# Optimization experiments

Hardware: AMD Instinct MI355X
Metric: run time of the kernel (lower is better)

The kernel has to match this reference:

```python
import jax, jax.numpy as jnp
import numpy as np

B, L = 8, 2048          # images, lines per image
C_IN, HW = 256, 128     # backbone feature channels, spatial size
DIM_LOI = 128
N_PTS0, N_PTS1 = 32, 8  # sampled points per line, after maxpool
SCALE = N_PTS0 // N_PTS1
EPS = 1e-5


def setup_inputs() -> dict:
    key = jax.random.key(0)
    ks = jax.random.split(key, 24)
    d = {}
    d['feature'] = jax.random.normal(ks[0], (B, C_IN, HW, HW), jnp.float32)
    # line endpoints in pixel coords [0, 128)
    d['lines'] = jax.random.uniform(ks[1], (B, L, 2, 2), jnp.float32) * HW
    # fc1: 1x1 conv 256 -> 128
    d['fc1_w'] = jax.random.normal(ks[2], (DIM_LOI, C_IN), jnp.float32) * 0.05
    d['fc1_b'] = jnp.zeros((DIM_LOI,), jnp.float32)
    planes = DIM_LOI // 2
    def bn(k, c):
        k1, k2, k3 = jax.random.split(k, 3)
        return (jax.random.normal(k1, (c,), jnp.float32) * 0.1 + 1.0,
                jax.random.normal(k2, (c,), jnp.float32) * 0.1,
                jax.random.normal(k3, (c,), jnp.float32) * 0.05,
                jax.random.uniform(jax.random.fold_in(k, 7), (c,), jnp.float32, 0.5, 1.5))
    d['bn1_g'], d['bn1_b'], d['bn1_m'], d['bn1_v'] = bn(ks[3], DIM_LOI)
    d['conv1_w'] = jax.random.normal(ks[4], (planes, DIM_LOI), jnp.float32) * 0.05
    d['conv1_b'] = jnp.zeros((planes,), jnp.float32)
    d['bn2_g'], d['bn2_b'], d['bn2_m'], d['bn2_v'] = bn(ks[5], planes)
    d['conv2_w'] = jax.random.normal(ks[6], (planes, planes, 3), jnp.float32) * 0.05
    d['conv2_b'] = jnp.zeros((planes,), jnp.float32)
    d['bn3_g'], d['bn3_b'], d['bn3_m'], d['bn3_v'] = bn(ks[7], planes)
    d['conv3_w'] = jax.random.normal(ks[8], (DIM_LOI, planes), jnp.float32) * 0.05
    d['conv3_b'] = jnp.zeros((DIM_LOI,), jnp.float32)
    d['fc2_w'] = jax.random.normal(ks[9], (1, DIM_LOI * N_PTS1), jnp.float32) * 0.02
    d['fc2_b'] = jnp.zeros((1,), jnp.float32)
    return d


def _bn(x, g, b, m, v):
    # x: [N, C, T], eval-mode batchnorm
    s = g * jax.lax.rsqrt(v + EPS)
    return x * s[None, :, None] + (b - m * s)[None, :, None]


def _loi_forward(feature, lines, fc1_w, fc1_b,
                 bn1_g, bn1_b, bn1_m, bn1_v, conv1_w, conv1_b,
                 bn2_g, bn2_b, bn2_m, bn2_v, conv2_w, conv2_b,
                 bn3_g, bn3_b, bn3_m, bn3_v, conv3_w, conv3_b,
                 fc2_w, fc2_b):
    # fc1: 1x1 conv -> [B, DIM_LOI, H, W]
    x = jnp.einsum('oc,bchw->bohw', fc1_w, feature) + fc1_b[None, :, None, None]

    # sample N_PTS0 points per line: p = p0*lam + p1*(1-lam) - 0.5
    lam = jnp.linspace(0.0, 1.0, N_PTS0, dtype=lines.dtype)  # [P]
    pts = (lines[:, :, 0, None, :] * lam[None, None, :, None]
           + lines[:, :, 1, None, :] * (1.0 - lam[None, None, :, None]) - 0.5)  # [B,L,P,2]
    px, py = pts[..., 0], pts[..., 1]
    px0 = jnp.clip(jnp.floor(px), 0.0, HW - 1.0)
    py0 = jnp.clip(jnp.floor(py), 0.0, HW - 1.0)
    px1 = jnp.clip(px0 + 1.0, 0.0, HW - 1.0)
    py1 = jnp.clip(py0 + 1.0, 0.0, HW - 1.0)
    px0l, py0l = px0.astype(jnp.int32), py0.astype(jnp.int32)
    px1l, py1l = px1.astype(jnp.int32), py1.astype(jnp.int32)

    def gather(f, ix, iy):  # f: [C,H,W], ix/iy: [L,P] -> [C,L,P]
        return f[:, ix, iy]

    gat = jax.vmap(gather)  # over batch
    xp = (gat(x, px0l, py0l) * ((px1 - px) * (py1 - py))[:, None]
          + gat(x, px1l, py0l) * ((px - px0) * (py1 - py))[:, None]
          + gat(x, px0l, py1l) * ((px1 - px) * (py - py0))[:, None]
          + gat(x, px1l, py1l) * ((px - px0) * (py - py0))[:, None])  # [B,C,L,P]

    xp = xp.transpose(0, 2, 1, 3).reshape(B * L, DIM_LOI, N_PTS0)  # [N,C,P]
    # MaxPool1d(kernel=stride=SCALE)
    xp = xp.reshape(B * L, DIM_LOI, N_PTS1, SCALE).max(axis=-1)  # [N,C,T=8]

    # Bottleneck1D residual: x + op(x)
    h = jax.nn.relu(_bn(xp, bn1_g, bn1_b, bn1_m, bn1_v))
    h = jnp.einsum('oc,nct->not', conv1_w, h) + conv1_b[None, :, None]
    h = jax.nn.relu(_bn(h, bn2_g, bn2_b, bn2_m, bn2_v))
    h = jax.lax.conv_general_dilated(h, conv2_w, (1,), [(1, 1)],
                                     dimension_numbers=('NCH', 'OIH', 'NCH'))
    h = h + conv2_b[None, :, None]
    h = jax.nn.relu(_bn(h, bn3_g, bn3_b, bn3_m, bn3_v))
    h = jnp.einsum('oc,nct->not', conv3_w, h) + conv3_b[None, :, None]
    xp = xp + h

    # fc2: ReLU -> Linear(dim_loi*n_pts1, 1)
    flat = jax.nn.relu(xp).reshape(B * L, DIM_LOI * N_PTS1)
    logits = (flat @ fc2_w.T + fc2_b).reshape(-1)  # [B*L]
    return logits


def reference(feature, lines, fc1_w, fc1_b,
              bn1_g, bn1_b, bn1_m, bn1_v, conv1_w, conv1_b,
              bn2_g, bn2_b, bn2_m, bn2_v, conv2_w, conv2_b,
              bn3_g, bn3_b, bn3_m, bn3_v, conv3_w, conv3_b,
              fc2_w, fc2_b):
    return _loi_forward(feature, lines, fc1_w, fc1_b,
                        bn1_g, bn1_b, bn1_m, bn1_v, conv1_w, conv1_b,
                        bn2_g, bn2_b, bn2_m, bn2_v, conv2_w, conv2_b,
                        bn3_g, bn3_b, bn3_m, bn3_v, conv3_w, conv3_b,
                        fc2_w, fc2_b)
```

## Files before the change

### kernel.cpp

```cpp
#include <hip/hip_runtime.h>

#define EPSBN 1e-5f

typedef _Float16 f16;
typedef _Float16 f16x8 __attribute__((ext_vector_type(8)));
typedef _Float16 f16x4 __attribute__((ext_vector_type(4)));
typedef _Float16 f16x2 __attribute__((ext_vector_type(2)));
typedef float    f32x4 __attribute__((ext_vector_type(4)));

#define AS1 __attribute__((address_space(1)))
#define AS3 __attribute__((address_space(3)))

__device__ inline f16x8 hmax8(f16x8 a, f16x8 b) {
    f16x8 r;
    #pragma unroll
    for (int i = 0; i < 8; ++i) r[i] = a[i] > b[i] ? a[i] : b[i];
    return r;
}
__device__ inline f16x8 relu8(f16x8 v) {
    f16x8 r;
    #pragma unroll
    for (int i = 0; i < 8; ++i) r[i] = v[i] > (f16)0.f ? v[i] : (f16)0.f;
    return r;
}

__global__ void wprep_kernel(const float* __restrict__ fc1w,
                             const float* __restrict__ w1,
                             const float* __restrict__ w2,
                             const float* __restrict__ w3,
                             f16* __restrict__ dst) {
    const int i = blockIdx.x * 256 + threadIdx.x;
    float v;
    if (i < 32768) {
        const int k8 = i & 7, otg = (i >> 3) & 7, l = (i >> 6) & 63, s = i >> 12;
        const int n16l = l & 15, quadl = l >> 4;
        v = fc1w[(otg * 16 + n16l) * 256 + s * 32 + quadl * 8 + k8];
    }
    else if (i < 40960) v = w1[i - 32768];
    else if (i < 53248) {
        const int j = i - 40960, tau = j >> 12, rest = j & 4095;
        v = w2[rest * 3 + tau];
    } else              v = w3[i - 53248];
    dst[i] = (f16)v;
}

__global__ __launch_bounds__(1024, 4)
void fc1_mfma(const float* __restrict__ feat,
              const f16*   __restrict__ wfrag,
              const float* __restrict__ bias,
              f16*         __restrict__ xmap) {
    __shared__ f16 wlds[32768];
    __shared__ union {
        f16 xb[2][32][264];
        f16 epi[128][132];
    } u;

    const int tid  = threadIdx.x;
    const int wv   = tid >> 6;
    const int lane = tid & 63;
    const int n16  = lane & 15, quad = lane >> 4;
    const int pw   = wv >> 1;
    const int ow   = wv & 1;
    const int img  = blockIdx.x & 7;
    const int p0   = (blockIdx.x >> 3) << 8;

    const float* fimg = feat + (((size_t)img) << 22);

    const int sch = tid >> 5, sg = tid & 31;
    const float* sbase = fimg + (((size_t)sch) << 14) + p0 + sg * 8;

    f32x4 acc[2][4];
    #pragma unroll
    for (int ptg = 0; ptg < 2; ++ptg)
        #pragma unroll
        for (int t = 0; t < 4; ++t) acc[ptg][t] = (f32x4){0.f, 0.f, 0.f, 0.f};

    #pragma unroll
    for (int c4 = 0; c4 < 4; ++c4) {
        const int c = wv + 16 * c4;
        __builtin_amdgcn_global_load_lds((const AS1 void*)(wfrag + c * 512 + lane * 8),
                                         (AS3 void*)(wlds + c * 512), 16, 0, 0);
    }
    float4 st[2][2];
    st[0][0] = *(const float4*)(sbase);
    st[0][1] = *(const float4*)(sbase + 4);
    st[1][0] = *(const float4*)(sbase + 524288);
    st[1][1] = *(const float4*)(sbase + 524292);
    {
        f16x8 h;
        #pragma unroll
        for (int i = 0; i < 4; ++i) { h[i] = (f16)st[0][0][i]; h[i + 4] = (f16)st[0][1][i]; }
        *(f16x8*)&u.xb[0][sch][sg * 8] = h;
    }
    asm volatile("s_waitcnt vmcnt(0)" ::: "memory");
    __syncthreads();

    #pragma unroll
    for (int s = 0; s < 8; ++s) {
        if (s < 6) {
            st[s & 1][0] = *(const float4*)(sbase + (size_t)(s + 2) * 524288);
            st[s & 1][1] = *(const float4*)(sbase + (size_t)(s + 2) * 524288 + 4);
        }

        f16x8 wf[4];
        #pragma unroll
        for (int t = 0; t < 4; ++t)
            wf[t] = *(const f16x8*)&wlds[((s * 64 + lane) * 8 + ow * 4 + t) * 8];

        f16x8 xf[2];
        #pragma unroll
        for (int ptg = 0; ptg < 2; ++ptg) {
            const int pt = pw * 32 + ptg * 16 + n16;
            f16x8 xv;
            #pragma unroll
            for (int j = 0; j < 8; ++j) xv[j] = u.xb[s & 1][quad * 8 + j][pt];
            xf[ptg] = xv;
        }

        #pragma unroll
        for (int ptg = 0; ptg < 2; ++ptg)
            #pragma unroll
            for (int t = 0; t < 4; ++t)
                acc[ptg][t] = __builtin_amdgcn_mfma_f32_16x16x32_f16(wf[t], xf[ptg],
                                                                     acc[ptg][t], 0, 0, 0);

        if (s < 7) {
            f16x8 h;
            #pragma unroll
            for (int i = 0; i < 4; ++i) {
                h[i]     = (f16)st[(s + 1) & 1][0][i];
                h[i + 4] = (f16)st[(s + 1) & 1][1][i];
            }
            *(f16x8*)&u.xb[(s + 1) & 1][sch][sg * 8] = h;

            __builtin_amdgcn_sched_barrier(0);
            asm volatile("s_waitcnt lgkmcnt(0)" ::: "memory");
            __builtin_amdgcn_sched_barrier(0);
            __builtin_amdgcn_s_barrier();
            __builtin_amdgcn_sched_barrier(0);
        }
    }

    #pragma unroll
    for (int P = 0; P < 2; ++P) {
        __syncthreads();
        if ((pw >> 2) == P) {
            #pragma unroll
            for (int ptg = 0; ptg < 2; ++ptg) {
                const int rowl = (pw & 3) * 32 + ptg * 16 + n16;
                #pragma unroll
                for (int t = 0; t < 4; ++t) {
                    const int o = ow * 64 + t * 16 + quad * 4;
                    const float4 bq = *(const float4*)&bias[o];
                    f16x4 hv;
                    hv[0] = (f16)(acc[ptg][t][0] + bq.x);
                    hv[1] = (f16)(acc[ptg][t][1] + bq.y);
                    hv[2] = (f16)(acc[ptg][t][2] + bq.z);
                    hv[3] = (f16)(acc[ptg][t][3] + bq.w);
                    *(f16x4*)&u.epi[rowl][o] = hv;
                }
            }
        }
        __syncthreads();
        #pragma unroll
        for (int it = 0; it < 2; ++it) {
            const int idx = it * 1024 + tid;
            const int rowl = idx >> 4, seg = idx & 15;
            const float4 v = *(const float4*)&u.epi[rowl][seg * 8];
            *(float4*)&xmap[(((size_t)(img * 16384 + p0 + P * 128 + rowl)) << 7) + seg * 8] = v;
        }
    }
}

__global__ __launch_bounds__(256)
void loi_kernel(const f16*   __restrict__ x,
                const float* __restrict__ lines,
                const f16*   __restrict__ wsp,
                const float* __restrict__ bn1g, const float* __restrict__ bn1b,
                const float* __restrict__ bn1m, const float* __restrict__ bn1v,
                const float* __restrict__ b1,
                const float* __restrict__ bn2g, const float* __restrict__ bn2b,
                const float* __restrict__ bn2m, const float* __restrict__ bn2v,
                const float* __restrict__ b2,
                const float* __restrict__ bn3g, const float* __restrict__ bn3b,
                const float* __restrict__ bn3m, const float* __restrict__ bn3v,
                const float* __restrict__ b3,
                const float* __restrict__ fc2w, const float* __restrict__ fc2b,
                float* __restrict__ out) {
    __shared__ f16 xp[64][136];
    __shared__ alignas(16) union {
        struct { int toff[256][4]; f16 twgt[256][4]; } tp;
        struct { f16 h1[80][72]; f16 h2[64][72]; } cv;
    } u;
    __shared__ f16 s1h[128], t1h[128];
    __shared__ float s2f[64], t2f[64], s3f[64], t3f[64], b1f[64], b2f[64];
    __shared__ float b3f[128];
    __shared__ float wsum[4][8];

    const f16* w1f16 = wsp + 32768;
    const f16* w2f16 = wsp + 40960;
    const f16* w3f16 = wsp + 53248;

    const int tid  = threadIdx.x;
    const int wv   = tid >> 6, lane = tid & 63;
    const int n16  = lane & 15, quad = lane >> 4;
    const int img  = blockIdx.x & 7;
    const int mblk = blockIdx.x >> 3;

    if (tid < 128) {
        const float s = bn1g[tid] * rsqrtf(bn1v[tid] + EPSBN);
        s1h[tid] = (f16)s; t1h[tid] = (f16)(bn1b[tid] - bn1m[tid] * s);
    }
    if (tid < 64) {
        const float s = bn2g[tid] * rsqrtf(bn2v[tid] + EPSBN);
        s2f[tid] = s; t2f[tid] = bn2b[tid] - bn2m[tid] * s;
        b1f[tid] = b1[tid];
    } else if (tid < 128) {
        const int c = tid - 64;
        const float s = bn3g[c] * rsqrtf(bn3v[c] + EPSBN);
        s3f[c] = s; t3f[c] = bn3b[c] - bn3m[c] * s;
        b2f[c] = b2[c];
    } else {
        b3f[tid - 128] = b3[tid - 128];
    }

    {
        const int li = tid >> 5, pt = tid & 31;
        const int gl = img * 2048 + mblk * 8 + li;
        const float4 ln = *(const float4*)&lines[gl * 4];
        const float lam = (float)pt * (1.0f / 31.0f);
        const float px = ln.x * lam + ln.z * (1.f - lam) - 0.5f;
        const float py = ln.y * lam + ln.w * (1.f - lam) - 0.5f;
        const float px0 = fminf(fmaxf(floorf(px), 0.f), 127.f);
        const float py0 = fminf(fmaxf(floorf(py), 0.f), 127.f);
        const float px1 = fminf(px0 + 1.f, 127.f);
        const float py1 = fminf(py0 + 1.f, 127.f);
        const int ix0 = (int)px0, iy0 = (int)py0;
        const int ix1 = (int)px1, iy1 = (int)py1;
        u.tp.toff[tid][0] = (((ix0 << 7) + iy0) << 7);
        u.tp.toff[tid][1] = (((ix1 << 7) + iy0) << 7);
        u.tp.toff[tid][2] = (((ix0 << 7) + iy1) << 7);
        u.tp.toff[tid][3] = (((ix1 << 7) + iy1) << 7);
        const float wx1 = px1 - px, wx0 = px - px0;
        const float wy1 = py1 - py, wy0 = py - py0;
        u.tp.twgt[tid][0] = (f16)(wx1 * wy1); u.tp.twgt[tid][1] = (f16)(wx0 * wy1);
        u.tp.twgt[tid][2] = (f16)(wx1 * wy0); u.tp.twgt[tid][3] = (f16)(wx0 * wy0);
    }
    __syncthreads();

    {
        const int h  = lane >> 5;
        const int sh = (lane >> 4) & 1;
        const int j  = lane & 15;
        const int li = wv * 2 + h;
        const f16* xbh = x + (((size_t)img) << 21) + 8 * j;
        #pragma unroll
        for (int t = 0; t < 8; ++t) {
            f16x8 m;
            #pragma unroll
            for (int q = 0; q < 8; ++q) m[q] = (f16)(-60000.f);
            #pragma unroll
            for (int ss = 0; ss < 2; ++ss) {
                const int combo = li * 32 + t * 4 + sh * 2 + ss;
                const int4  off = *(const int4*)&u.tp.toff[combo][0];
                const f16x4 tw  = *(const f16x4*)&u.tp.twgt[combo][0];
                const f16x8 g00 = *(const f16x8*)(xbh + off.x);
                const f16x8 g10 = *(const f16x8*)(xbh + off.y);
                const f16x8 g01 = *(const f16x8*)(xbh + off.z);
                const f16x8 g11 = *(const f16x8*)(xbh + off.w);
                f16x8 w0, w1v, w2v, w3v;
                #pragma unroll
                for (int q = 0; q < 8; ++q) {
                    w0[q] = tw[0]; w1v[q] = tw[1]; w2v[q] = tw[2]; w3v[q] = tw[3];
                }
                const f16x8 v = g00 * w0 + g10 * w1v + g01 * w2v + g11 * w3v;
                m = hmax8(m, v);
            }
            union { f16x8 v8; int i4[4]; } cv;
            cv.v8 = m;
            #pragma unroll
            for (int q = 0; q < 4; ++q) cv.i4[q] = __shfl_xor(cv.i4[q], 16, 64);
            m = hmax8(m, cv.v8);
            if (sh == 0) *(f16x8*)&xp[li * 8 + t][8 * j] = m;
        }
    }
    __syncthreads();

    {
        const int r = tid >> 4, seg = tid & 15;
        const int row = (r >> 1) * 10 + (r & 1) * 9;
        *(unsigned long long*)&u.cv.h1[row][seg * 4] = 0ull;
    }

    {
        const int o_lane = wv * 16 + n16;
        f32x4 acc1[4];
        #pragma unroll
        for (int nt = 0; nt < 4; ++nt) acc1[nt] = (f32x4){0.f, 0.f, 0.f, 0.f};
        #pragma unroll
        for (int ks = 0; ks < 4; ++ks) {
            const int k = ks * 32 + quad * 8;
            const f16x8 a  = *(const f16x8*)&w1f16[o_lane * 128 + k];
            const f16x8 s8 = *(const f16x8*)&s1h[k];
            const f16x8 t8 = *(const f16x8*)&t1h[k];
            #pragma unroll
            for (int nt = 0; nt < 4; ++nt) {
                const f16x8 raw = *(const f16x8*)&xp[nt * 16 + n16][k];
                const f16x8 bf = relu8(raw * s8 + t8);
                acc1[nt] = __builtin_amdgcn_mfma_f32_16x16x32_f16(a, bf, acc1[nt], 0, 0, 0);
            }
        }
        #pragma unroll
        for (int nt = 0; nt < 4; ++nt) {
            const int n = nt * 16 + n16;
            const int nprow = (n >> 3) * 10 + (n & 7) + 1;
            #pragma unroll
            for (int r = 0; r < 4; ++r) {
                const int o = wv * 16 + quad * 4 + r;
                const float v = fmaxf((acc1[nt][r] + b1f[o]) * s2f[o] + t2f[o], 0.f);
                u.cv.h1[nprow][o] = (f16)v;
            }
        }
    }
    __syncthreads();

    {
        const int o_lane = wv * 16 + n16;
        f32x4 acc2[4];
        #pragma unroll
        for (int nt = 0; nt < 4; ++nt) acc2[nt] = (f32x4){0.f, 0.f, 0.f, 0.f};
        #pragma unroll
        for (int d = 0; d < 3; ++d) {
            const f16* A2 = w2f16 + d * 4096;
            #pragma unroll
            for (int ks = 0; ks < 2; ++ks) {
                const int k = ks * 32 + quad * 8;
                const f16x8 a = *(const f16x8*)&A2[o_lane * 64 + k];
                #pragma unroll
                for (int nt = 0; nt < 4; ++nt) {
                    const int n = nt * 16 + n16;
                    const int row = (n >> 3) * 10 + (n & 7) + d;
                    const f16x8 bf = *(const f16x8*)&u.cv.h1[row][k];
                    acc2[nt] = __builtin_amdgcn_mfma_f32_16x16x32_f16(a, bf, acc2[nt], 0, 0, 0);
                }
            }
        }
        #pragma unroll
        for (int nt = 0; nt < 4; ++nt) {
            const int n = nt * 16 + n16;
            #pragma unroll
            for (int r = 0; r < 4; ++r) {
                const int o = wv * 16 + quad * 4 + r;
                const float v = fmaxf((acc2[nt][r] + b2f[o]) * s3f[o] + t3f[o], 0.f);
                u.cv.h2[n][o] = (f16)v;
            }
        }
    }
    __syncthreads();

    {
        const int col = n16 & 7, obase = wv * 16 + quad * 4;
        float fcv[2][4];
        #pragma unroll
        for (int h = 0; h < 2; ++h)
            #pragma unroll
            for (int r = 0; r < 4; ++r)
                fcv[h][r] = fc2w[(h * 64 + obase + r) * 8 + col];

        f32x4 acc3[2][4];
        #pragma unroll
        for (int h = 0; h < 2; ++h)
            #pragma unroll
            for (int nt = 0; nt < 4; ++nt) acc3[h][nt] = (f32x4){0.f, 0.f, 0.f, 0.f};
        #pragma unroll
        for (int ks = 0; ks < 2; ++ks) {
            const int k = ks * 32 + quad * 8;
            const f16x8 a0 = *(const f16x8*)&w3f16[(wv * 16 + n16) * 64 + k];
            const f16x8 a1 = *(const f16x8*)&w3f16[(64 + wv * 16 + n16) * 64 + k];
            #pragma unroll
            for (int nt = 0; nt < 4; ++nt) {
                const f16x8 bf = *(const f16x8*)&u.cv.h2[nt * 16 + n16][k];
                acc3[0][nt] = __builtin_amdgcn_mfma_f32_16x16x32_f16(a0, bf, acc3[0][nt], 0, 0, 0);
                acc3[1][nt] = __builtin_amdgcn_mfma_f32_16x16x32_f16(a1, bf, acc3[1][nt], 0, 0, 0);
            }
        }
        float part[4] = {0.f, 0.f, 0.f, 0.f};
        #pragma unroll
        for (int h = 0; h < 2; ++h) {
            const float4 bq = *(const float4*)&b3f[h * 64 + obase];
            const float bqa[4] = {bq.x, bq.y, bq.z, bq.w};
            #pragma unroll
            for (int nt = 0; nt < 4; ++nt) {
                const int n = nt * 16 + n16;
                const f16x4 rx = *(const f16x4*)&xp[n][h * 64 + obase];
                float p = 0.f;
                #pragma unroll
                for (int r = 0; r < 4; ++r) {
                    float v = acc3[h][nt][r] + bqa[r] + (float)rx[r];
                    v = fmaxf(v, 0.f);
                    p += v * fcv[h][r];
                }
                part[nt] += p;
            }
        }
        #pragma unroll
        for (int off_i = 0; off_i < 5; ++off_i) {
            const int off = (int[]){1, 2, 4, 16, 32}[off_i];
            part[0] += __shfl_xor(part[0], off, 64);
            part[1] += __shfl_xor(part[1], off, 64);
            part[2] += __shfl_xor(part[2], off, 64);
            part[3] += __shfl_xor(part[3], off, 64);
        }
        if ((lane & 55) == 0) {
            const int par = (lane >> 3) & 1;
            wsum[wv][0 + par] = part[0];
            wsum[wv][2 + par] = part[1];
            wsum[wv][4 + par] = part[2];
            wsum[wv][6 + par] = part[3];
        }
    }
    __syncthreads();

    if (tid < 8) {
        const float s = wsum[0][tid] + wsum[1][tid] + wsum[2][tid] + wsum[3][tid];
        out[img * 2048 + mblk * 8 + tid] = s + fc2b[0];
    }
}

extern "C" void kernel_launch(void* const* d_in, const int* in_sizes, int n_in,
                              void* d_out, int out_size, void* d_ws, size_t ws_size,
                              hipStream_t stream) {
    const float* feature = (const float*)d_in[0];
    const float* lines   = (const float*)d_in[1];
    const float* fc1_w   = (const float*)d_in[2];
    const float* fc1_b   = (const float*)d_in[3];
    const float* bn1g    = (const float*)d_in[4];
    const float* bn1b    = (const float*)d_in[5];
    const float* bn1m    = (const float*)d_in[6];
    const float* bn1v    = (const float*)d_in[7];
    const float* w1      = (const float*)d_in[8];
    const float* b1      = (const float*)d_in[9];
    const float* bn2g    = (const float*)d_in[10];
    const float* bn2b    = (const float*)d_in[11];
    const float* bn2m    = (const float*)d_in[12];
    const float* bn2v    = (const float*)d_in[13];
    const float* w2      = (const float*)d_in[14];
    const float* b2      = (const float*)d_in[15];
    const float* bn3g    = (const float*)d_in[16];
    const float* bn3b    = (const float*)d_in[17];
    const float* bn3m    = (const float*)d_in[18];
    const float* bn3v    = (const float*)d_in[19];
    const float* w3      = (const float*)d_in[20];
    const float* b3      = (const float*)d_in[21];
    const float* fc2w    = (const float*)d_in[22];
    const float* fc2b    = (const float*)d_in[23];

    f16* xmap = (f16*)d_ws;
    f16* wsp  = (f16*)((char*)d_ws + (size_t)32 * 1024 * 1024);

    wprep_kernel<<<240, 256, 0, stream>>>(fc1_w, w1, w2, w3, wsp);
    fc1_mfma<<<512, 1024, 0, stream>>>(feature, wsp, fc1_b, xmap);
    loi_kernel<<<2048, 256, 0, stream>>>(xmap, lines, wsp,
                                         bn1g, bn1b, bn1m, bn1v, b1,
                                         bn2g, bn2b, bn2m, bn2v, b2,
                                         bn3g, bn3b, bn3m, bn3v, b3,
                                         fc2w, fc2b, (float*)d_out);
}
```

Before: 283.0 us.

## Transpose fc1 activation staging to point-major swizzled LDS and reorder weight fragments

The fc1 MFMA kernel now stages features in LDS as [point][channel] with an XOR swizzle. Each lane can then read its 8-channel MFMA B fragment with one 16-byte LDS load instead of eight strided scalar loads. The cost is that global loads become scalar per-channel reads rather than float4 vectors, though they still coalesce across threads. Weight fragments are reordered so each lane's LDS reads are contiguous per wave, and the epilogue uses a smaller 64-row padded buffer written out in four passes.

```diff
diff --git a/kernel.cpp b/kernel.cpp
--- a/kernel.cpp
+++ b/kernel.cpp
@@ -32,9 +32,13 @@
     const int i = blockIdx.x * 256 + threadIdx.x;
     float v;
     if (i < 32768) {
-        const int k8 = i & 7, otg = (i >> 3) & 7, l = (i >> 6) & 63, s = i >> 12;
-        const int n16l = l & 15, quadl = l >> 4;
-        v = fc1w[(otg * 16 + n16l) * 256 + s * 32 + quadl * 8 + k8];
+        const int k8   = i & 7;
+        const int lane = (i >> 3) & 63;
+        const int t    = (i >> 9) & 3;
+        const int ow   = (i >> 11) & 1;
+        const int s    = (i >> 12) & 7;
+        const int n16l = lane & 15, quadl = lane >> 4;
+        v = fc1w[(ow * 64 + t * 16 + n16l) * 256 + s * 32 + quadl * 8 + k8];
     }
     else if (i < 40960) v = w1[i - 32768];
     else if (i < 53248) {
@@ -51,8 +55,8 @@
               f16*         __restrict__ xmap) {
     __shared__ f16 wlds[32768];
     __shared__ union {
-        f16 xb[2][32][264];
-        f16 epi[128][132];
+        f16 xb[2][256][32];
+        f16 epi[64][136];
     } u;
 
     const int tid  = threadIdx.x;
@@ -66,8 +70,9 @@
 
     const float* fimg = feat + (((size_t)img) << 22);
 
-    const int sch = tid >> 5, sg = tid & 31;
-    const float* sbase = fimg + (((size_t)sch) << 14) + p0 + sg * 8;
+    const int spt = tid & 255, chgrp = tid >> 8;
+    const float* sbase = fimg + (((size_t)(chgrp * 8)) << 14) + p0 + spt;
+    const int swcol = (chgrp ^ ((spt >> 1) & 3)) << 3;
 
     f32x4 acc[2][4];
     #pragma unroll
@@ -81,16 +86,17 @@
         __builtin_amdgcn_global_load_lds((const AS1 void*)(wfrag + c * 512 + lane * 8),
                                          (AS3 void*)(wlds + c * 512), 16, 0, 0);
     }
-    float4 st[2][2];
-    st[0][0] = *(const float4*)(sbase);
-    st[0][1] = *(const float4*)(sbase + 4);
-    st[1][0] = *(const float4*)(sbase + 524288);
-    st[1][1] = *(const float4*)(sbase + 524292);
+    float st[2][8];
+    #pragma unroll
+    for (int c = 0; c < 8; ++c) {
+        st[0][c] = sbase[(size_t)c << 14];
+        st[1][c] = sbase[524288 + ((size_t)c << 14)];
+    }
     {
         f16x8 h;
         #pragma unroll
-        for (int i = 0; i < 4; ++i) { h[i] = (f16)st[0][0][i]; h[i + 4] = (f16)st[0][1][i]; }
-        *(f16x8*)&u.xb[0][sch][sg * 8] = h;
+        for (int c = 0; c < 8; ++c) h[c] = (f16)st[0][c];
+        *(f16x8*)&u.xb[0][spt][swcol] = h;
     }
     asm volatile("s_waitcnt vmcnt(0)" ::: "memory");
     __syncthreads();
@@ -98,23 +104,21 @@
     #pragma unroll
     for (int s = 0; s < 8; ++s) {
         if (s < 6) {
-            st[s & 1][0] = *(const float4*)(sbase + (size_t)(s + 2) * 524288);
-            st[s & 1][1] = *(const float4*)(sbase + (size_t)(s + 2) * 524288 + 4);
+            #pragma unroll
+            for (int c = 0; c < 8; ++c)
+                st[s & 1][c] = sbase[(size_t)(s + 2) * 524288 + ((size_t)c << 14)];
         }
 
         f16x8 wf[4];
         #pragma unroll
         for (int t = 0; t < 4; ++t)
-            wf[t] = *(const f16x8*)&wlds[((s * 64 + lane) * 8 + ow * 4 + t) * 8];
+            wf[t] = *(const f16x8*)&wlds[((((s * 2 + ow) * 4 + t) * 64) + lane) * 8];
 
         f16x8 xf[2];
         #pragma unroll
         for (int ptg = 0; ptg < 2; ++ptg) {
             const int pt = pw * 32 + ptg * 16 + n16;
-            f16x8 xv;
-            #pragma unroll
-            for (int j = 0; j < 8; ++j) xv[j] = u.xb[s & 1][quad * 8 + j][pt];
-            xf[ptg] = xv;
+            xf[ptg] = *(const f16x8*)&u.xb[s & 1][pt][(quad ^ ((pt >> 1) & 3)) << 3];
         }
 
         #pragma unroll
@@ -127,11 +131,8 @@
         if (s < 7) {
             f16x8 h;
             #pragma unroll
-            for (int i = 0; i < 4; ++i) {
-                h[i]     = (f16)st[(s + 1) & 1][0][i];
-                h[i + 4] = (f16)st[(s + 1) & 1][1][i];
-            }
-            *(f16x8*)&u.xb[(s + 1) & 1][sch][sg * 8] = h;
+            for (int c = 0; c < 8; ++c) h[c] = (f16)st[(s + 1) & 1][c];
+            *(f16x8*)&u.xb[(s + 1) & 1][spt][swcol] = h;
 
             __builtin_amdgcn_sched_barrier(0);
             asm volatile("s_waitcnt lgkmcnt(0)" ::: "memory");
@@ -142,12 +143,12 @@
     }
 
     #pragma unroll
-    for (int P = 0; P < 2; ++P) {
+    for (int P = 0; P < 4; ++P) {
         __syncthreads();
-        if ((pw >> 2) == P) {
+        if ((pw >> 1) == P) {
             #pragma unroll
             for (int ptg = 0; ptg < 2; ++ptg) {
-                const int rowl = (pw & 3) * 32 + ptg * 16 + n16;
+                const int rowl = (pw & 1) * 32 + ptg * 16 + n16;
                 #pragma unroll
                 for (int t = 0; t < 4; ++t) {
                     const int o = ow * 64 + t * 16 + quad * 4;
@@ -162,12 +163,10 @@
             }
         }
         __syncthreads();
-        #pragma unroll
-        for (int it = 0; it < 2; ++it) {
-            const int idx = it * 1024 + tid;
-            const int rowl = idx >> 4, seg = idx & 15;
+        {
+            const int rowl = tid >> 4, seg = tid & 15;
             const float4 v = *(const float4*)&u.epi[rowl][seg * 8];
-            *(float4*)&xmap[(((size_t)(img * 16384 + p0 + P * 128 + rowl)) << 7) + seg * 8] = v;
+            *(float4*)&xmap[(((size_t)(img * 16384 + p0 + P * 64 + rowl)) << 7) + seg * 8] = v;
         }
     }
 }
```

New measurement: 278.1 us. No clear change (-1.7%).
